# Kernel optimization log

Hardware: AMD Instinct MI355X
Metric: run time of the kernel (lower is better)

## Reference

```python
import jax, jax.numpy as jnp
import numpy as np

EPS_IN = 1e-5   # InstanceNorm2d default eps
EPS_VAR = 1e-6  # clamp on attention variance

def instance_norm(x):
    # x: (b, c, h, w); affine=False, biased variance over spatial dims
    mean = jnp.mean(x, axis=(2, 3), keepdims=True)
    var = jnp.var(x, axis=(2, 3), keepdims=True)
    return (x - mean) * jax.lax.rsqrt(var + EPS_IN)

def setup_inputs() -> dict:
    key = jax.random.key(0)
    k1, k2, k3, k4 = jax.random.split(key, 4)
    shp = (4, 512, 64, 64)
    return {
        "c_x": jax.random.normal(k1, shp, dtype=jnp.float32),
        "s_x": jax.random.normal(k2, shp, dtype=jnp.float32),
        "c_1x": jax.random.normal(k3, shp, dtype=jnp.float32),
        "s_1x": jax.random.normal(k4, shp, dtype=jnp.float32),
    }

def reference(c_x, s_x, c_1x, s_1x):
    b, v_dim, h, w = c_x.shape
    hw = h * w
    # Q: (b, hw, qk), K: (b, qk, hw), V: (b, hw, v)
    Q = instance_norm(c_1x).reshape(b, -1, hw).transpose(0, 2, 1)
    K = instance_norm(s_1x).reshape(b, -1, s_1x.shape[2] * s_1x.shape[3])
    V = s_x.reshape(b, v_dim, -1).transpose(0, 2, 1)
    # attention over spatial tokens
    A = jax.nn.softmax(jnp.einsum('bqc,bck->bqk', Q, K), axis=-1)
    M = jnp.einsum('bqk,bkv->bqv', A, V)              # weighted mean
    Var = jnp.einsum('bqk,bkv->bqv', A, V * V) - M * M  # weighted variance
    S = jnp.sqrt(jnp.clip(Var, EPS_VAR, None))
    # back to (b, v, h, w)
    M = M.reshape(b, h, w, -1).transpose(0, 3, 1, 2)
    S = S.reshape(b, h, w, -1).transpose(0, 3, 1, 2)
    return S * instance_norm(c_x) + M
```

## Files before the change

### kernel.cpp

```cpp
#include <hip/hip_runtime.h>
#include <cmath>


#define B_  4
#define C_  512
#define HW_ 4096

typedef _Float16 f16;
typedef _Float16 f16x8 __attribute__((ext_vector_type(8)));
typedef float    f32x4 __attribute__((ext_vector_type(4)));

__device__ __forceinline__ f32x4 mfma16(f16x8 a, f16x8 b, f32x4 c) {
  return __builtin_amdgcn_mfma_f32_16x16x32_f16(a, b, c, 0, 0, 0);
}
__device__ __forceinline__ void g2l16(const f16* g, f16* l) {
  __builtin_amdgcn_global_load_lds(
      (const __attribute__((address_space(1))) void*)g,
      (__attribute__((address_space(3))) void*)l, 16, 0, 0);
}

__global__ __launch_bounds__(256) void k_stats(
    const float* __restrict__ cx, const float* __restrict__ c1,
    const float* __restrict__ s1,
    float2* __restrict__ cxs, float2* __restrict__ c1s, float2* __restrict__ s1s) {
  int c = blockIdx.x, b = blockIdx.y, t = blockIdx.z;
  const float* src = (t == 0 ? cx : (t == 1 ? c1 : s1)) + (size_t)(b * C_ + c) * HW_;
  float s = 0.f, q = 0.f;
  const float4* src4 = (const float4*)src;
  for (int i = threadIdx.x; i < HW_ / 4; i += 256) {
    float4 v = src4[i];
    s += v.x + v.y + v.z + v.w;
    q += v.x * v.x + v.y * v.y + v.z * v.z + v.w * v.w;
  }
#pragma unroll
  for (int off = 1; off < 64; off <<= 1) {
    s += __shfl_xor(s, off);
    q += __shfl_xor(q, off);
  }
  __shared__ float ss[4], sq[4];
  int wv = threadIdx.x >> 6;
  if ((threadIdx.x & 63) == 0) { ss[wv] = s; sq[wv] = q; }
  __syncthreads();
  if (threadIdx.x == 0) {
    float S = ss[0] + ss[1] + ss[2] + ss[3];
    float Q = sq[0] + sq[1] + sq[2] + sq[3];
    float mean = S * (1.f / HW_);
    float var = Q * (1.f / HW_) - mean * mean;
    float2 r;
    r.x = mean;
    r.y = rsqrtf(var + 1e-5f);
    (t == 0 ? cxs : (t == 1 ? c1s : s1s))[b * C_ + c] = r;
  }
}

__global__ __launch_bounds__(256) void k_prept(
    const float* __restrict__ src, const float2* __restrict__ st,
    f16* __restrict__ dst) {
  int pb = blockIdx.x * 64, cb = blockIdx.y * 64, b = blockIdx.z;
  __shared__ float t[64][65];
  int tj = threadIdx.x & 63, tr = threadIdx.x >> 6;
#pragma unroll 4
  for (int p = 0; p < 16; ++p) {
    int cl = p * 4 + tr;
    float2 mr = st[b * C_ + cb + cl];
    float v = src[(size_t)(b * C_ + cb + cl) * HW_ + pb + tj];
    t[cl][tj] = (v - mr.x) * mr.y;
  }
  __syncthreads();
#pragma unroll 4
  for (int p = 0; p < 16; ++p) {
    int pr = p * 4 + tr;
    dst[(size_t)(b * HW_ + pb + pr) * C_ + cb + tj] = (f16)t[tj][pr];
  }
}

__global__ __launch_bounds__(256) void k_prepv(const float* __restrict__ src,
                                               f16* __restrict__ dst) {
  int gid = blockIdx.x * 256 + threadIdx.x;
  const float4* s = (const float4*)src + (size_t)gid * 2;
  float4 v0 = s[0], v1 = s[1];
  f16x8 v = {(f16)v0.x, (f16)v0.y, (f16)v0.z, (f16)v0.w,
             (f16)v1.x, (f16)v1.y, (f16)v1.z, (f16)v1.w};
  *(f16x8*)(dst + (size_t)gid * 8) = v;
}

__global__ __launch_bounds__(256, 2) void k_qk(
    const f16* __restrict__ Qt, const f16* __restrict__ Kt,
    f16* __restrict__ E, float2* __restrict__ mlpart,
    int qspan, int qt128, int npair) {
  int id = blockIdx.x, pair, kt;
  if ((npair & 7) == 0) {
    int xcd = id & 7, j = id >> 3, qrs = npair >> 3;
    pair = xcd * qrs + (j % qrs);
    kt = j / qrs;
  } else {
    pair = id >> 4;
    kt = id & 15;
  }
  int bz = pair / qt128, qt = pair - bz * qt128;

  const f16* Aq = Qt + ((size_t)(bz * qspan + qt * 128)) * C_;
  const f16* Bk = Kt + (size_t)bz * HW_ * C_ + (size_t)kt * 256 * C_;
  f16* Eb = E + ((size_t)(bz * qspan + qt * 128)) * HW_ + kt * 256;
  float2* mlb = mlpart + ((size_t)(bz * qspan + qt * 128)) * 16 + kt;

  __shared__ __align__(16) union ShQK {
    struct { f16 As[128 * 32]; f16 Bs[256 * 32]; } s;
    f16 ebuf[32 * 272];
  } sh;
  __shared__ float sred[2][128];
  f16* As = sh.s.As;
  f16* Bs = sh.s.Bs;

  int t = threadIdx.x, wave = t >> 6, lane = t & 63, lq = lane & 15, quad = lane >> 4;
  int wy = wave >> 1, wx = wave & 1;
  int srow = t >> 2, scol = (t & 3) * 8;

  f32x4 acc[4][8];
#pragma unroll
  for (int mt = 0; mt < 4; ++mt)
#pragma unroll
    for (int nt = 0; nt < 8; ++nt) acc[mt][nt] = (f32x4){0, 0, 0, 0};

  for (int kc = 0; kc < 16; ++kc) {
    __syncthreads();
    g2l16(Aq + (size_t)srow * C_ + kc * 32 + scol, As + t * 8);
    g2l16(Aq + (size_t)(srow + 64) * C_ + kc * 32 + scol, As + 2048 + t * 8);
#pragma unroll
    for (int i = 0; i < 4; ++i)
      g2l16(Bk + (size_t)(srow + 64 * i) * C_ + kc * 32 + scol,
            Bs + i * 2048 + t * 8);
    __syncthreads();
    f16x8 af[4], bf[8];
#pragma unroll
    for (int mt = 0; mt < 4; ++mt)
      af[mt] = *(const f16x8*)(As + (wy * 64 + mt * 16 + lq) * 32 + quad * 8);
#pragma unroll
    for (int nt = 0; nt < 8; ++nt)
      bf[nt] = *(const f16x8*)(Bs + (wx * 128 + nt * 16 + lq) * 32 + quad * 8);
#pragma unroll
    for (int mt = 0; mt < 4; ++mt)
#pragma unroll
      for (int nt = 0; nt < 8; ++nt)
        acc[mt][nt] = mfma16(af[mt], bf[nt], acc[mt][nt]);
  }

#pragma unroll
  for (int mt = 0; mt < 4; ++mt)
#pragma unroll
    for (int r = 0; r < 4; ++r) {
      float v = -1e30f;
#pragma unroll
      for (int nt = 0; nt < 8; ++nt) v = fmaxf(v, acc[mt][nt][r]);
#pragma unroll
      for (int msk = 1; msk < 16; msk <<= 1) v = fmaxf(v, __shfl_xor(v, msk));
      if (lq == 0) sred[wx][wy * 64 + mt * 16 + quad * 4 + r] = v;
    }
  __syncthreads();
  float mrow[4][4];
#pragma unroll
  for (int mt = 0; mt < 4; ++mt)
#pragma unroll
    for (int r = 0; r < 4; ++r) {
      int rr = wy * 64 + mt * 16 + quad * 4 + r;
      mrow[mt][r] = fmaxf(sred[0][rr], sred[1][rr]);
    }

  float rsum[4][4];
#pragma unroll
  for (int mt = 0; mt < 4; ++mt)
#pragma unroll
    for (int r = 0; r < 4; ++r) rsum[mt][r] = 0.f;

#pragma unroll
  for (int mt = 0; mt < 4; ++mt) {
    __syncthreads();
#pragma unroll
    for (int nt = 0; nt < 8; ++nt) {
      f32x4 v = acc[mt][nt];
#pragma unroll
      for (int r = 0; r < 4; ++r) {
        float e = __expf(v[r] - mrow[mt][r]);
        rsum[mt][r] += e;
        sh.ebuf[(wy * 16 + quad * 4 + r) * 272 + wx * 128 + nt * 16 + lq] = (f16)e;
      }
    }
    __syncthreads();
#pragma unroll
    for (int i = 0; i < 4; ++i) {
      int idx = i * 256 + t;
      int rl = idx >> 5, cs = (idx & 31) * 8;
      f16x8 v8 = *(const f16x8*)(sh.ebuf + rl * 272 + cs);
      int grow = (rl >> 4) * 64 + mt * 16 + (rl & 15);
      *(f16x8*)(Eb + (size_t)grow * HW_ + cs) = v8;
    }
  }

#pragma unroll
  for (int mt = 0; mt < 4; ++mt)
#pragma unroll
    for (int r = 0; r < 4; ++r) {
      float v = rsum[mt][r];
#pragma unroll
      for (int msk = 1; msk < 16; msk <<= 1) v += __shfl_xor(v, msk);
      if (lq == 0) sred[wx][wy * 64 + mt * 16 + quad * 4 + r] = v;
    }
  __syncthreads();
  if (wx == 0 && lq == 0) {
#pragma unroll
    for (int mt = 0; mt < 4; ++mt)
#pragma unroll
      for (int r = 0; r < 4; ++r) {
        int rr = wy * 64 + mt * 16 + quad * 4 + r;
        mlb[(size_t)rr * 16] = make_float2(mrow[mt][r], sred[0][rr] + sred[1][rr]);
      }
  }
}

__global__ __launch_bounds__(256) void k_red(const float2* __restrict__ mlpart,
                                             float* __restrict__ alpha) {
  int row = blockIdx.x * 256 + threadIdx.x;
  const float2* p = mlpart + (size_t)row * 16;
  float2 loc[16];
  float m = -1e30f;
#pragma unroll
  for (int i = 0; i < 16; ++i) {
    loc[i] = p[i];
    m = fmaxf(m, loc[i].x);
  }
  float l = 0.f;
#pragma unroll
  for (int i = 0; i < 16; ++i) l += loc[i].y * __expf(loc[i].x - m);
  float invl = 1.f / l;
#pragma unroll
  for (int i = 0; i < 16; ++i)
    alpha[(size_t)row * 16 + i] = __expf(loc[i].x - m) * invl;
}

#define PV_STAGE_A(i)                                                         \
  g2l16(Ap + (size_t)((i)*64 + srow) * HW_ + s2 * 64 + scol,                  \
        sm + pnOff + (i)*4096 + t * 8)
#define PV_STAGE_B(i)                                                         \
  g2l16(Bv + (size_t)((i)*64 + srow) * HW_ + s2 * 64 + scol,                  \
        sm + pnOff + 16384 + (i)*4096 + t * 8)

#define PV_PHASE(CX, STAGE_STMT, POST_STMT)                                   \
  {                                                                           \
    f16x8 af0 = *(const f16x8*)(As_s + aoff + 0 * 1024 + (CX));               \
    f16x8 af1 = *(const f16x8*)(As_s + aoff + 1 * 1024 + (CX));               \
    f16x8 af2 = *(const f16x8*)(As_s + aoff + 2 * 1024 + (CX));               \
    f16x8 af3 = *(const f16x8*)(As_s + aoff + 3 * 1024 + (CX));               \
    f16x8 bf0 = *(const f16x8*)(Bs_s + boff + 0 * 1024 + (CX));               \
    f16x8 bf1 = *(const f16x8*)(Bs_s + boff + 1 * 1024 + (CX));               \
    f16x8 bf2 = *(const f16x8*)(Bs_s + boff + 2 * 1024 + (CX));               \
    f16x8 bf3 = *(const f16x8*)(Bs_s + boff + 3 * 1024 + (CX));               \
    STAGE_STMT;                                                               \
    asm volatile("s_waitcnt lgkmcnt(0)" ::: "memory");                        \
    __builtin_amdgcn_sched_barrier(0);                                        \
    __builtin_amdgcn_s_setprio(1);                                            \
    af0 *= aal[0]; af1 *= aal[1]; af2 *= aal[2]; af3 *= aal[3];               \
    f16x8 q0 = bf0 * bf0, q1 = bf1 * bf1, q2 = bf2 * bf2, q3 = bf3 * bf3;     \
    accM [0][0] = mfma16(af0, bf0, accM [0][0]);                              \
    accM2[0][0] = mfma16(af0, q0,  accM2[0][0]);                              \
    accM [0][1] = mfma16(af0, bf1, accM [0][1]);                              \
    accM2[0][1] = mfma16(af0, q1,  accM2[0][1]);                              \
    accM [0][2] = mfma16(af0, bf2, accM [0][2]);                              \
    accM2[0][2] = mfma16(af0, q2,  accM2[0][2]);                              \
    accM [0][3] = mfma16(af0, bf3, accM [0][3]);                              \
    accM2[0][3] = mfma16(af0, q3,  accM2[0][3]);                              \
    accM [1][0] = mfma16(af1, bf0, accM [1][0]);                              \
    accM2[1][0] = mfma16(af1, q0,  accM2[1][0]);                              \
    accM [1][1] = mfma16(af1, bf1, accM [1][1]);                              \
    accM2[1][1] = mfma16(af1, q1,  accM2[1][1]);                              \
    accM [1][2] = mfma16(af1, bf2, accM [1][2]);                              \
    accM2[1][2] = mfma16(af1, q2,  accM2[1][2]);                              \
    accM [1][3] = mfma16(af1, bf3, accM [1][3]);                              \
    accM2[1][3] = mfma16(af1, q3,  accM2[1][3]);                              \
    accM [2][0] = mfma16(af2, bf0, accM [2][0]);                              \
    accM2[2][0] = mfma16(af2, q0,  accM2[2][0]);                              \
    accM [2][1] = mfma16(af2, bf1, accM [2][1]);                              \
    accM2[2][1] = mfma16(af2, q1,  accM2[2][1]);                              \
    accM [2][2] = mfma16(af2, bf2, accM [2][2]);                              \
    accM2[2][2] = mfma16(af2, q2,  accM2[2][2]);                              \
    accM [2][3] = mfma16(af2, bf3, accM [2][3]);                              \
    accM2[2][3] = mfma16(af2, q3,  accM2[2][3]);                              \
    accM [3][0] = mfma16(af3, bf0, accM [3][0]);                              \
    accM2[3][0] = mfma16(af3, q0,  accM2[3][0]);                              \
    accM [3][1] = mfma16(af3, bf1, accM [3][1]);                              \
    accM2[3][1] = mfma16(af3, q1,  accM2[3][1]);                              \
    accM [3][2] = mfma16(af3, bf2, accM [3][2]);                              \
    accM2[3][2] = mfma16(af3, q2,  accM2[3][2]);                              \
    accM [3][3] = mfma16(af3, bf3, accM [3][3]);                              \
    accM2[3][3] = mfma16(af3, q3,  accM2[3][3]);                              \
    __builtin_amdgcn_s_setprio(0);                                            \
    POST_STMT;                                                                \
  }

__global__ __launch_bounds__(512, 2) void k_pv(
    const f16* __restrict__ P, const float* __restrict__ alphaG,
    const f16* __restrict__ V, const float* __restrict__ cx,
    const float2* __restrict__ cxs, float* __restrict__ out,
    int qspan, int qbase, int qt256) {
  int npairs = (int)gridDim.x >> 2;
  int id = blockIdx.x, pair, ct;
  if ((npairs & 7) == 0) {
    int x = id & 7, j = id >> 3, ppx = npairs >> 3;
    pair = x * ppx + (j >> 2);
    ct = j & 3;
  } else {
    pair = id >> 2;
    ct = id & 3;
  }
  int bz = pair / qt256, qt = pair - bz * qt256;

  const f16* Ap = P + ((size_t)(bz * qspan + qt * 256)) * HW_;
  const f16* Bv = V + ((size_t)(bz * C_ + ct * 128)) * HW_;

  __shared__ __align__(16) f16 sm[3 * 24576 + 256 * 17];
  f16* Alh = sm + 3 * 24576;

  int t = threadIdx.x, wave = t >> 6, lane = t & 63, lq = lane & 15, quad = lane >> 4;
  int wy = wave >> 1, wx = wave & 1;

  {
    const float* ag = alphaG + ((size_t)(bz * qspan + qt * 256)) * 16;
#pragma unroll
    for (int i = 0; i < 8; ++i) {
      int e = i * 512 + t;
      Alh[(e >> 4) * 17 + (e & 15)] = (f16)ag[e];
    }
  }

  int srow = t >> 3;
  int scol = ((t & 7) ^ (srow & 7)) * 8;

  int aoff = (wy * 64 + lq) * 64;
  int boff = (wx * 64 + lq) * 64;
  int cx0 = (quad * 8) ^ ((lq & 7) << 3);
  int cx1 = (32 + quad * 8) ^ ((lq & 7) << 3);

  f32x4 accM[4][4], accM2[4][4];
#pragma unroll
  for (int mt = 0; mt < 4; ++mt)
#pragma unroll
    for (int nt = 0; nt < 4; ++nt) {
      accM[mt][nt] = (f32x4){0, 0, 0, 0};
      accM2[mt][nt] = (f32x4){0, 0, 0, 0};
    }

#pragma unroll
  for (int s0 = 0; s0 < 2; ++s0) {
    int off = s0 * 24576;
#pragma unroll
    for (int i = 0; i < 4; ++i)
      g2l16(Ap + (size_t)(i * 64 + srow) * HW_ + s0 * 64 + scol,
            sm + off + i * 4096 + t * 8);
#pragma unroll
    for (int i = 0; i < 2; ++i)
      g2l16(Bv + (size_t)(i * 64 + srow) * HW_ + s0 * 64 + scol,
            sm + off + 16384 + i * 4096 + t * 8);
  }
  asm volatile("s_waitcnt lgkmcnt(0)" ::: "memory");
  asm volatile("s_waitcnt vmcnt(6)" ::: "memory");
  __builtin_amdgcn_s_barrier();

  int ph = 0, pn = 2;
  for (int s = 0; s < 64; ++s) {
    const f16* As_s = sm + ph * 24576;
    const f16* Bs_s = As_s + 16384;
    int pnOff = pn * 24576;
    int s2 = s + 2;
    bool st = s < 62;
    int ktl = s >> 2;
    f16 aal[4];
    aal[0] = Alh[(wy * 64 + lq +  0) * 17 + ktl];
    aal[1] = Alh[(wy * 64 + lq + 16) * 17 + ktl];
    aal[2] = Alh[(wy * 64 + lq + 32) * 17 + ktl];
    aal[3] = Alh[(wy * 64 + lq + 48) * 17 + ktl];

    PV_PHASE(cx0,
             if (st) { PV_STAGE_A(0); PV_STAGE_A(1); PV_STAGE_A(2); }, )
    PV_PHASE(cx1,
             if (st) { PV_STAGE_A(3); PV_STAGE_B(0); PV_STAGE_B(1); },
             if (st) { asm volatile("s_waitcnt vmcnt(6)" ::: "memory"); }
             else    { asm volatile("s_waitcnt vmcnt(0)" ::: "memory"); })
    __builtin_amdgcn_s_barrier();

    ph = (ph == 2) ? 0 : ph + 1;
    pn = (pn == 2) ? 0 : pn + 1;
  }

  int chbase = ct * 128 + wx * 64;
#pragma unroll
  for (int mt = 0; mt < 4; ++mt) {
    int q0 = qbase + qt * 256 + wy * 64 + mt * 16 + quad * 4;
#pragma unroll
    for (int nt = 0; nt < 4; ++nt) {
      int c = chbase + nt * 16 + lq;
      float2 stc = cxs[bz * C_ + c];
      size_t base = ((size_t)bz * C_ + c) * HW_ + q0;
      float4 cv = *(const float4*)(cx + base);
      f32x4 m1 = accM[mt][nt], m2 = accM2[mt][nt];
      float4 o;
      o.x = sqrtf(fmaxf(m2[0] - m1[0] * m1[0], 1e-6f)) * ((cv.x - stc.x) * stc.y) + m1[0];
      o.y = sqrtf(fmaxf(m2[1] - m1[1] * m1[1], 1e-6f)) * ((cv.y - stc.x) * stc.y) + m1[1];
      o.z = sqrtf(fmaxf(m2[2] - m1[2] * m1[2], 1e-6f)) * ((cv.z - stc.x) * stc.y) + m1[2];
      o.w = sqrtf(fmaxf(m2[3] - m1[3] * m1[3], 1e-6f)) * ((cv.w - stc.x) * stc.y) + m1[3];
      *(float4*)(out + base) = o;
    }
  }
}

extern "C" void kernel_launch(void* const* d_in, const int* in_sizes, int n_in,
                              void* d_out, int out_size, void* d_ws,
                              size_t ws_size, hipStream_t stream) {
  const float* c_x = (const float*)d_in[0];
  const float* s_x = (const float*)d_in[1];
  const float* c1x = (const float*)d_in[2];
  const float* s1x = (const float*)d_in[3];
  float* out = (float*)d_out;

  char* ws = (char*)d_ws;
  size_t o = 0;
  f16* Qt = (f16*)(ws + o);  o += (size_t)B_ * HW_ * C_ * 2;
  f16* Kt = (f16*)(ws + o);  o += (size_t)B_ * HW_ * C_ * 2;
  f16* Vh = (f16*)(ws + o);  o += (size_t)B_ * HW_ * C_ * 2;
  float2* cxs = (float2*)(ws + o); o += B_ * C_ * sizeof(float2);
  float2* c1s = (float2*)(ws + o); o += B_ * C_ * sizeof(float2);
  float2* s1s = (float2*)(ws + o); o += B_ * C_ * sizeof(float2);
  size_t fixed = (o + 255) & ~(size_t)255;

  const size_t per_row = (size_t)HW_ * 2 + 16 * 8 + 16 * 4;
  struct Cfg { int nb, qs; };
  const Cfg cfgs[5] = {{4, 4096}, {1, 4096}, {1, 2048}, {1, 1024}, {1, 512}};
  Cfg cfg = cfgs[4];
  for (int i = 0; i < 5; ++i) {
    size_t rows = (size_t)cfgs[i].nb * cfgs[i].qs;
    if (fixed + rows * per_row <= ws_size) { cfg = cfgs[i]; break; }
  }
  const int nb = cfg.nb, qspan = cfg.qs, qt128 = qspan / 128, qt256 = qspan / 256;
  const int npair = nb * qt128;
  const int npv = nb * qt256;
  const size_t rows = (size_t)nb * qspan;
  f16* E = (f16*)(ws + fixed);
  float2* mlpart = (float2*)(ws + fixed + rows * HW_ * 2);
  float* alpha = (float*)(ws + fixed + rows * HW_ * 2 + rows * 16 * 4 * 2);

  k_stats<<<dim3(C_, B_, 3), 256, 0, stream>>>(c_x, c1x, s1x, cxs, c1s, s1s);
  k_prept<<<dim3(HW_ / 64, C_ / 64, B_), 256, 0, stream>>>(c1x, c1s, Qt);
  k_prept<<<dim3(HW_ / 64, C_ / 64, B_), 256, 0, stream>>>(s1x, s1s, Kt);
  k_prepv<<<dim3(B_ * C_ * HW_ / 8 / 256), 256, 0, stream>>>(s_x, Vh);

  for (int b0 = 0; b0 < B_; b0 += nb) {
    for (int qb = 0; qb < HW_; qb += qspan) {
      const f16* Qtp = Qt + ((size_t)b0 * HW_ + qb) * C_;
      const f16* Ktp = Kt + (size_t)b0 * HW_ * C_;
      const f16* Vp = Vh + (size_t)b0 * C_ * HW_;
      const float* cxp = c_x + (size_t)b0 * C_ * HW_;
      const float2* cxsp = cxs + b0 * C_;
      float* outp = out + (size_t)b0 * C_ * HW_;

      k_qk<<<dim3((unsigned)(npair * 16)), 256, 0, stream>>>(
          Qtp, Ktp, E, mlpart, qspan, qt128, npair);
      k_red<<<dim3((unsigned)(rows / 256)), 256, 0, stream>>>(mlpart, alpha);
      k_pv<<<dim3((unsigned)(npv * 4)), 512, 0, stream>>>(
          E, alpha, Vp, cxp, cxsp, outp, qspan, qb, qt256);
    }
  }
}
```

Measured before the change: 387.0 us.

## Enlarge QK tile to 256 rows with triple-buffered async LDS pipeline

The QK^T softmax-numerator kernel now uses 512-thread blocks covering 256 query rows by 256 keys, and replaces the load-then-compute loop with a three-slot LDS ring. Global-to-LDS loads are issued two stages ahead, with vmcnt waits and raw barriers in place of paired __syncthreads. It also raises wave priority around the MFMA burst and XOR-swizzles the exp staging buffer to cut LDS bank conflicts. The aim is to hide global load latency and halve K re-reads per query. The cost is much larger LDS use (about 96KB plus sred), which may allow only one block per CU despite the launch bound of 2.

```diff
diff --git a/kernel.cpp b/kernel.cpp
--- a/kernel.cpp
+++ b/kernel.cpp
@@ -84,10 +84,10 @@
   *(f16x8*)(dst + (size_t)gid * 8) = v;
 }
 
-__global__ __launch_bounds__(256, 2) void k_qk(
+__global__ __launch_bounds__(512, 2) void k_qk(
     const f16* __restrict__ Qt, const f16* __restrict__ Kt,
     f16* __restrict__ E, float2* __restrict__ mlpart,
-    int qspan, int qt128, int npair) {
+    int qspan, int qt256, int npair) {
   int id = blockIdx.x, pair, kt;
   if ((npair & 7) == 0) {
     int xcd = id & 7, j = id >> 3, qrs = npair >> 3;
@@ -97,52 +97,80 @@
     pair = id >> 4;
     kt = id & 15;
   }
-  int bz = pair / qt128, qt = pair - bz * qt128;
-
-  const f16* Aq = Qt + ((size_t)(bz * qspan + qt * 128)) * C_;
+  int bz = pair / qt256, qt = pair - bz * qt256;
+
+  const f16* Aq = Qt + ((size_t)(bz * qspan + qt * 256)) * C_;
   const f16* Bk = Kt + (size_t)bz * HW_ * C_ + (size_t)kt * 256 * C_;
-  f16* Eb = E + ((size_t)(bz * qspan + qt * 128)) * HW_ + kt * 256;
-  float2* mlb = mlpart + ((size_t)(bz * qspan + qt * 128)) * 16 + kt;
+  f16* Eb = E + ((size_t)(bz * qspan + qt * 256)) * HW_ + kt * 256;
+  float2* mlb = mlpart + ((size_t)(bz * qspan + qt * 256)) * 16 + kt;
 
   __shared__ __align__(16) union ShQK {
-    struct { f16 As[128 * 32]; f16 Bs[256 * 32]; } s;
-    f16 ebuf[32 * 272];
+    f16 ring[3 * 16384];
+    f16 ebuf[64 * 272];
   } sh;
-  __shared__ float sred[2][128];
-  f16* As = sh.s.As;
-  f16* Bs = sh.s.Bs;
+  __shared__ float sred[2][256];
 
   int t = threadIdx.x, wave = t >> 6, lane = t & 63, lq = lane & 15, quad = lane >> 4;
   int wy = wave >> 1, wx = wave & 1;
   int srow = t >> 2, scol = (t & 3) * 8;
 
+  int aoff = (wy * 64 + lq) * 32 + quad * 8;
+  int boff = (wx * 128 + lq) * 32 + quad * 8;
+
   f32x4 acc[4][8];
 #pragma unroll
   for (int mt = 0; mt < 4; ++mt)
 #pragma unroll
     for (int nt = 0; nt < 8; ++nt) acc[mt][nt] = (f32x4){0, 0, 0, 0};
 
-  for (int kc = 0; kc < 16; ++kc) {
-    __syncthreads();
-    g2l16(Aq + (size_t)srow * C_ + kc * 32 + scol, As + t * 8);
-    g2l16(Aq + (size_t)(srow + 64) * C_ + kc * 32 + scol, As + 2048 + t * 8);
-#pragma unroll
-    for (int i = 0; i < 4; ++i)
-      g2l16(Bk + (size_t)(srow + 64 * i) * C_ + kc * 32 + scol,
-            Bs + i * 2048 + t * 8);
-    __syncthreads();
+#pragma unroll
+  for (int s0 = 0; s0 < 2; ++s0) {
+    int off = s0 * 16384;
+    g2l16(Aq + (size_t)srow * C_ + s0 * 32 + scol, sh.ring + off + t * 8);
+    g2l16(Aq + (size_t)(128 + srow) * C_ + s0 * 32 + scol, sh.ring + off + 4096 + t * 8);
+    g2l16(Bk + (size_t)srow * C_ + s0 * 32 + scol, sh.ring + off + 8192 + t * 8);
+    g2l16(Bk + (size_t)(128 + srow) * C_ + s0 * 32 + scol, sh.ring + off + 12288 + t * 8);
+  }
+  asm volatile("s_waitcnt vmcnt(4)" ::: "memory");
+  __builtin_amdgcn_s_barrier();
+
+  int cur = 0, pn = 2;
+  for (int s = 0; s < 16; ++s) {
+    const f16* As_s = sh.ring + cur * 16384;
+    const f16* Bs_s = As_s + 8192;
+    int pnOff = pn * 16384;
+    bool st = s < 14;
+
     f16x8 af[4], bf[8];
 #pragma unroll
     for (int mt = 0; mt < 4; ++mt)
-      af[mt] = *(const f16x8*)(As + (wy * 64 + mt * 16 + lq) * 32 + quad * 8);
+      af[mt] = *(const f16x8*)(As_s + aoff + mt * 512);
 #pragma unroll
     for (int nt = 0; nt < 8; ++nt)
-      bf[nt] = *(const f16x8*)(Bs + (wx * 128 + nt * 16 + lq) * 32 + quad * 8);
+      bf[nt] = *(const f16x8*)(Bs_s + boff + nt * 512);
+
+    if (st) {
+      int c2 = (s + 2) * 32;
+      g2l16(Aq + (size_t)srow * C_ + c2 + scol, sh.ring + pnOff + t * 8);
+      g2l16(Aq + (size_t)(128 + srow) * C_ + c2 + scol, sh.ring + pnOff + 4096 + t * 8);
+      g2l16(Bk + (size_t)srow * C_ + c2 + scol, sh.ring + pnOff + 8192 + t * 8);
+      g2l16(Bk + (size_t)(128 + srow) * C_ + c2 + scol, sh.ring + pnOff + 12288 + t * 8);
+    }
+    asm volatile("s_waitcnt lgkmcnt(0)" ::: "memory");
+    __builtin_amdgcn_sched_barrier(0);
+    __builtin_amdgcn_s_setprio(1);
 #pragma unroll
     for (int mt = 0; mt < 4; ++mt)
 #pragma unroll
       for (int nt = 0; nt < 8; ++nt)
         acc[mt][nt] = mfma16(af[mt], bf[nt], acc[mt][nt]);
+    __builtin_amdgcn_s_setprio(0);
+    if (st) { asm volatile("s_waitcnt vmcnt(4)" ::: "memory"); }
+    else    { asm volatile("s_waitcnt vmcnt(0)" ::: "memory"); }
+    __builtin_amdgcn_s_barrier();
+
+    cur = (cur == 2) ? 0 : cur + 1;
+    pn = (pn == 2) ? 0 : pn + 1;
   }
 
 #pragma unroll
@@ -178,21 +206,23 @@
 #pragma unroll
     for (int nt = 0; nt < 8; ++nt) {
       f32x4 v = acc[mt][nt];
+      int cs = ((wx * 16 + nt * 2 + (lq >> 3)) ^ (quad << 1)) * 8 + (lq & 7);
 #pragma unroll
       for (int r = 0; r < 4; ++r) {
         float e = __expf(v[r] - mrow[mt][r]);
         rsum[mt][r] += e;
-        sh.ebuf[(wy * 16 + quad * 4 + r) * 272 + wx * 128 + nt * 16 + lq] = (f16)e;
+        sh.ebuf[(wy * 16 + quad * 4 + r) * 272 + cs] = (f16)e;
       }
     }
     __syncthreads();
 #pragma unroll
     for (int i = 0; i < 4; ++i) {
-      int idx = i * 256 + t;
-      int rl = idx >> 5, cs = (idx & 31) * 8;
-      f16x8 v8 = *(const f16x8*)(sh.ebuf + rl * 272 + cs);
+      int idx = i * 512 + t;
+      int rl = idx >> 5, ck = idx & 31;
+      int cr = (ck ^ (((rl >> 2) & 3) << 1)) * 8;
+      f16x8 v8 = *(const f16x8*)(sh.ebuf + rl * 272 + cr);
       int grow = (rl >> 4) * 64 + mt * 16 + (rl & 15);
-      *(f16x8*)(Eb + (size_t)grow * HW_ + cs) = v8;
+      *(f16x8*)(Eb + (size_t)grow * HW_ + ck * 8) = v8;
     }
   }
 
@@ -438,13 +468,12 @@
     size_t rows = (size_t)cfgs[i].nb * cfgs[i].qs;
     if (fixed + rows * per_row <= ws_size) { cfg = cfgs[i]; break; }
   }
-  const int nb = cfg.nb, qspan = cfg.qs, qt128 = qspan / 128, qt256 = qspan / 256;
-  const int npair = nb * qt128;
-  const int npv = nb * qt256;
+  const int nb = cfg.nb, qspan = cfg.qs, qt256 = qspan / 256;
+  const int npair256 = nb * qt256;
   const size_t rows = (size_t)nb * qspan;
   f16* E = (f16*)(ws + fixed);
   float2* mlpart = (float2*)(ws + fixed + rows * HW_ * 2);
-  float* alpha = (float*)(ws + fixed + rows * HW_ * 2 + rows * 16 * 4 * 2);
+  float* alpha = (float*)(ws + fixed + rows * HW_ * 2 + rows * 16 * 8);
 
   k_stats<<<dim3(C_, B_, 3), 256, 0, stream>>>(c_x, c1x, s1x, cxs, c1s, s1s);
   k_prept<<<dim3(HW_ / 64, C_ / 64, B_), 256, 0, stream>>>(c1x, c1s, Qt);
@@ -460,10 +489,10 @@
       const float2* cxsp = cxs + b0 * C_;
       float* outp = out + (size_t)b0 * C_ * HW_;
 
-      k_qk<<<dim3((unsigned)(npair * 16)), 256, 0, stream>>>(
-          Qtp, Ktp, E, mlpart, qspan, qt128, npair);
+      k_qk<<<dim3((unsigned)(npair256 * 16)), 512, 0, stream>>>(
+          Qtp, Ktp, E, mlpart, qspan, qt256, npair256);
       k_red<<<dim3((unsigned)(rows / 256)), 256, 0, stream>>>(mlpart, alpha);
-      k_pv<<<dim3((unsigned)(npv * 4)), 512, 0, stream>>>(
+      k_pv<<<dim3((unsigned)(npair256 * 4)), 512, 0, stream>>>(
           E, alpha, Vp, cxp, cxsp, outp, qspan, qb, qt256);
     }
   }
```

Result: no change. 386.4 us (-0.1%).
